# Kernel optimization log

Measured on AMD Instinct MI355X. Metric: run time of the kernel, lower is better.

The kernel has to match this reference:

```python
import jax, jax.numpy as jnp
import numpy as np

N = 50000      # nodes
E = 800000     # edges (before self-loops)
F_IN = 128     # num_features
HID = 32       # hidden_channels
HEADS = 4
CLS = 40       # num_classes
NEG_SLOPE = 0.2


def setup_inputs() -> dict:
    key = jax.random.key(0)
    ks = jax.random.split(key, 10)
    s = 0.1
    x = jax.random.normal(ks[0], (N, F_IN), jnp.float32)
    edge_index = jax.random.randint(ks[1], (2, E), 0, N, jnp.int32)
    W1 = jax.random.normal(ks[2], (F_IN, HEADS * HID), jnp.float32) * s
    att_src1 = jax.random.normal(ks[3], (HEADS, HID), jnp.float32) * s
    att_dst1 = jax.random.normal(ks[4], (HEADS, HID), jnp.float32) * s
    b1 = jnp.zeros((HEADS * HID,), jnp.float32)
    W2 = jax.random.normal(ks[5], (HEADS * HID, CLS), jnp.float32) * s
    att_src2 = jax.random.normal(ks[6], (1, CLS), jnp.float32) * s
    att_dst2 = jax.random.normal(ks[7], (1, CLS), jnp.float32) * s
    b2 = jnp.zeros((CLS,), jnp.float32)
    return {"x": x, "edge_index": edge_index,
            "W1": W1, "att_src1": att_src1, "att_dst1": att_dst1, "b1": b1,
            "W2": W2, "att_src2": att_src2, "att_dst2": att_dst2, "b2": b2}


def gat_layer(x, src, dst, W, a_src, a_dst, b, concat):
    """PyG GATConv: per-head linear, edge attention logits a_src.h_j + a_dst.h_i,
    LeakyReLU, segment softmax over incoming edges per dst, weighted scatter-sum."""
    n = x.shape[0]
    H, C = a_src.shape
    h = (x @ W).reshape(n, H, C)                       # [N, H, C]
    al_s = jnp.einsum('nhc,hc->nh', h, a_src)          # [N, H]
    al_d = jnp.einsum('nhc,hc->nh', h, a_dst)          # [N, H]
    e = jax.nn.leaky_relu(al_s[src] + al_d[dst], NEG_SLOPE)  # [E, H]
    e_max = jax.lax.stop_gradient(jax.ops.segment_max(e, dst, num_segments=n))
    e = jnp.exp(e - e_max[dst])
    denom = jax.ops.segment_sum(e, dst, num_segments=n)      # [N, H]
    alpha = e / (denom[dst] + 1e-16)                         # [E, H]
    out = jax.ops.segment_sum(h[src] * alpha[:, :, None], dst, num_segments=n)  # [N, H, C]
    out = out.reshape(n, H * C) if concat else out.mean(axis=1)
    return out + b


def reference(x, edge_index, W1, att_src1, att_dst1, b1, W2, att_src2, att_dst2, b2):
    n = x.shape[0]
    loops = jnp.arange(n, dtype=edge_index.dtype)
    src = jnp.concatenate([edge_index[0], loops])  # PyG adds self-loops by default
    dst = jnp.concatenate([edge_index[1], loops])
    h = gat_layer(x, src, dst, W1, att_src1, att_dst1, b1, concat=True)
    h = jax.nn.relu(h)  # dropout is identity in eval mode
    h = gat_layer(h, src, dst, W2, att_src2, att_dst2, b2, concat=False)
    return jax.nn.log_softmax(h, axis=1)
```

## Files before the change

### kernel.cpp

```cpp
#include <hip/hip_runtime.h>
#include <hip/hip_bf16.h>
#include <cstdint>
#include <cstddef>

#define NN 50000
#define EE 800000
#define FIN 128
#define D1 128
#define HEADS 4
#define HID 32
#define CLS 40
#define NEG 0.2f
#define MAXDEG 64
#define P2 128
#define PSZ2 391
#define CAP 8192
#define ABLK 400
#define ASLICE 500
#define GEMM1B 391

typedef __attribute__((ext_vector_type(8))) short short8;
typedef __attribute__((ext_vector_type(4))) float float4v;
typedef __attribute__((ext_vector_type(2))) float float2v;

union U16 { uint4 u; short8 s; };

__device__ __forceinline__ float bf2f(unsigned short u) {
    union { unsigned int i; float f; } v; v.i = ((unsigned int)u) << 16; return v.f;
}
__device__ __forceinline__ unsigned short f2bf(float f) {
    union { unsigned int i; float f; } v; v.f = f;
    unsigned int r = v.i + 0x7fffu + ((v.i >> 16) & 1u);
    return (unsigned short)(r >> 16);
}
__device__ __forceinline__ float2v up2(unsigned int u) {
    union { unsigned int i; float f; } lo, hi;
    lo.i = u << 16; hi.i = u & 0xffff0000u;
    float2v r; r[0] = lo.f; r[1] = hi.f; return r;
}

__global__ __launch_bounds__(256) void bucket_k(const int* __restrict__ eidx,
                                                unsigned int* __restrict__ seg,
                                                int* __restrict__ seg_cnt) {
    __shared__ int hist[P2], base_s[P2], run[P2];
    int t = threadIdx.x;
    if (t < P2) { hist[t] = 0; run[t] = 0; }
    __syncthreads();
    const int4* dst4 = (const int4*)(eidx + EE);
    const int4* src4 = (const int4*)eidx;
    int i0 = blockIdx.x * ASLICE;
    for (int i = i0 + t; i < i0 + ASLICE; i += 256) {
        int4 d = dst4[i];
        atomicAdd(&hist[d.x / PSZ2], 1);
        atomicAdd(&hist[d.y / PSZ2], 1);
        atomicAdd(&hist[d.z / PSZ2], 1);
        atomicAdd(&hist[d.w / PSZ2], 1);
    }
    __syncthreads();
    if (t < P2) base_s[t] = (hist[t] > 0) ? atomicAdd(&seg_cnt[t], hist[t]) : 0;
    __syncthreads();
    for (int i = i0 + t; i < i0 + ASLICE; i += 256) {
        int4 d = dst4[i];
        int4 s = src4[i];
        int p, off, idx;
        p = d.x / PSZ2; off = atomicAdd(&run[p], 1); idx = base_s[p] + off;
        if (idx < CAP) seg[(size_t)p * CAP + idx] = ((unsigned)s.x << 16) | (unsigned)(d.x - p * PSZ2);
        p = d.y / PSZ2; off = atomicAdd(&run[p], 1); idx = base_s[p] + off;
        if (idx < CAP) seg[(size_t)p * CAP + idx] = ((unsigned)s.y << 16) | (unsigned)(d.y - p * PSZ2);
        p = d.z / PSZ2; off = atomicAdd(&run[p], 1); idx = base_s[p] + off;
        if (idx < CAP) seg[(size_t)p * CAP + idx] = ((unsigned)s.z << 16) | (unsigned)(d.z - p * PSZ2);
        p = d.w / PSZ2; off = atomicAdd(&run[p], 1); idx = base_s[p] + off;
        if (idx < CAP) seg[(size_t)p * CAP + idx] = ((unsigned)s.w << 16) | (unsigned)(d.w - p * PSZ2);
    }
}

union BSM {
    struct { uint4 Wl[2048]; float sas[128]; float sad[128]; } g;
    int hist[PSZ2];
};

__global__ __launch_bounds__(256, 4) void bg_k(const unsigned int* __restrict__ seg,
                                               const int* __restrict__ seg_cnt,
                                               int* __restrict__ cnt,
                                               unsigned short* __restrict__ ssrcp,
                                               const float* __restrict__ X,
                                               const float* __restrict__ W,
                                               const float* __restrict__ as1,
                                               const float* __restrict__ ad1,
                                               unsigned int* __restrict__ H1b,
                                               float* __restrict__ ALS1,
                                               float* __restrict__ ALD1) {
    __shared__ BSM sm;
    int t = threadIdx.x;

    if (blockIdx.x < P2) {
        int p = blockIdx.x;
        int lo = p * PSZ2;
        int psz = min(PSZ2, NN - lo);
        for (int i = t; i < psz; i += 256) {
            sm.hist[i] = 1;
            ssrcp[(size_t)(lo + i) * MAXDEG] = (unsigned short)(lo + i);
        }
        __syncthreads();
        int m = min(seg_cnt[p], CAP);
        const unsigned int* sp = seg + (size_t)p * CAP;
        for (int i = t; i < m; i += 256) {
            unsigned int pr = sp[i];
            int dl  = (int)(pr & 0xffffu);
            int src = (int)(pr >> 16);
            int slot = atomicAdd(&sm.hist[dl], 1);
            if (slot < MAXDEG) ssrcp[(size_t)(lo + dl) * MAXDEG + slot] = (unsigned short)src;
        }
        __syncthreads();
        for (int i = t; i < psz; i += 256) cnt[lo + i] = sm.hist[i];
        return;
    }

    int bI = blockIdx.x - P2;
    if (t < 128) { sm.g.sas[t] = as1[t]; sm.g.sad[t] = ad1[t]; }
    for (int g = t; g < 2048; g += 256) {
        int ct = g >> 8, rem = g & 255, kc = rem >> 6, l = rem & 63;
        int c = ct * 16 + (l & 15);
        int k0 = kc * 32 + (l >> 4) * 8;
        U16 u;
#pragma unroll
        for (int j = 0; j < 8; j++) u.s[j] = (short)f2bf(W[(k0 + j) * D1 + c]);
        sm.g.Wl[g] = u.u;
    }
    __syncthreads();

    int wid = t >> 6, lane = t & 63, quad = lane >> 4, lrow = lane & 15;
    int wrow0 = bI * 128 + wid * 32;

    short8 afr[2][4];
#pragma unroll
    for (int rt = 0; rt < 2; rt++) {
        int r = wrow0 + rt * 16 + lrow;
#pragma unroll
        for (int kc = 0; kc < 4; kc++) {
            short8 a = {0, 0, 0, 0, 0, 0, 0, 0};
            if (r < NN) {
                const float* xp = X + (size_t)r * FIN + kc * 32 + quad * 8;
                float4 x0 = *(const float4*)xp;
                float4 x1 = *(const float4*)(xp + 4);
                a[0] = (short)f2bf(x0.x); a[1] = (short)f2bf(x0.y);
                a[2] = (short)f2bf(x0.z); a[3] = (short)f2bf(x0.w);
                a[4] = (short)f2bf(x1.x); a[5] = (short)f2bf(x1.y);
                a[6] = (short)f2bf(x1.z); a[7] = (short)f2bf(x1.w);
            }
            afr[rt][kc] = a;
        }
    }

    float4v acc[2][4];

    for (int cp = 0; cp < 2; ++cp) {
#pragma unroll
        for (int rt = 0; rt < 2; rt++)
#pragma unroll
            for (int c4 = 0; c4 < 4; c4++) acc[rt][c4] = (float4v)(0.f);

#pragma unroll
        for (int c4 = 0; c4 < 4; c4++) {
#pragma unroll
            for (int kc = 0; kc < 4; kc++) {
                U16 b; b.u = sm.g.Wl[((cp * 4 + c4) * 4 + kc) * 64 + lane];
                acc[0][c4] = __builtin_amdgcn_mfma_f32_16x16x32_bf16(afr[0][kc], b.s, acc[0][c4], 0, 0, 0);
                acc[1][c4] = __builtin_amdgcn_mfma_f32_16x16x32_bf16(afr[1][kc], b.s, acc[1][c4], 0, 0, 0);
            }
        }

#pragma unroll
        for (int rt = 0; rt < 2; rt++) {
#pragma unroll
            for (int reg = 0; reg < 4; reg++) {
                float ps[2] = {0.f, 0.f};
                float pd[2] = {0.f, 0.f};
#pragma unroll
                for (int c4 = 0; c4 < 4; c4++) {
                    float v = acc[rt][c4][reg];
                    int ct = cp * 4 + c4;
                    ps[c4 >> 1] += v * sm.g.sas[ct * 16 + lrow];
                    pd[c4 >> 1] += v * sm.g.sad[ct * 16 + lrow];
                }
#pragma unroll
                for (int o = 1; o < 16; o <<= 1) {
#pragma unroll
                    for (int h = 0; h < 2; h++) {
                        ps[h] += __shfl_xor(ps[h], o);
                        pd[h] += __shfl_xor(pd[h], o);
                    }
                }
                int r = wrow0 + rt * 16 + quad * 4 + reg;
                if (lrow == 0 && r < NN) {
                    *(float2*)&ALS1[(size_t)r * 4 + cp * 2] = make_float2(ps[0], ps[1]);
                    *(float2*)&ALD1[(size_t)r * 4 + cp * 2] = make_float2(pd[0], pd[1]);
                }
            }
        }

#pragma unroll
        for (int rt = 0; rt < 2; rt++)
#pragma unroll
            for (int c4 = 0; c4 < 4; c4++)
#pragma unroll
                for (int reg = 0; reg < 4; reg++) {
                    float v = acc[rt][c4][reg];
                    float o = __shfl_xor(v, 1);
                    int r = wrow0 + rt * 16 + quad * 4 + reg;
                    if (((lane & 1) == 0) && r < NN) {
                        unsigned int u = (unsigned int)f2bf(v) | ((unsigned int)f2bf(o) << 16);
                        H1b[(size_t)r * 64 + (cp * 4 + c4) * 8 + (lrow >> 1)] = u;
                    }
                }
    }
}

__global__ __launch_bounds__(256) void gather1_k(const int* __restrict__ cnt,
                                                 const unsigned short* __restrict__ ssrcp,
                                                 const uint4* __restrict__ H1b4,
                                                 const float4* __restrict__ ALS,
                                                 const float4* __restrict__ ALD,
                                                 const float* __restrict__ b1,
                                                 uint4* __restrict__ OUT1b4) {
    __shared__ float wlds[4][MAXDEG][4];
    __shared__ int sidlds[4][MAXDEG];
    int wid = threadIdx.x >> 6, lane = threadIdx.x & 63;
    int v = blockIdx.x * 4 + wid;
    int deg = min(cnt[v], MAXDEG);
    float4 ad = ALD[v];
    float w0 = 0.f, w1 = 0.f, w2 = 0.f, w3 = 0.f;
    if (lane < deg) {
        int s = (int)ssrcp[(size_t)v * MAXDEG + lane];
        sidlds[wid][lane] = s;
        float4 as = ALS[s];
        float l0 = as.x + ad.x; l0 = l0 > 0.f ? l0 : NEG * l0;
        float l1 = as.y + ad.y; l1 = l1 > 0.f ? l1 : NEG * l1;
        float l2 = as.z + ad.z; l2 = l2 > 0.f ? l2 : NEG * l2;
        float l3 = as.w + ad.w; l3 = l3 > 0.f ? l3 : NEG * l3;
        w0 = __expf(l0); w1 = __expf(l1); w2 = __expf(l2); w3 = __expf(l3);
        wlds[wid][lane][0] = w0; wlds[wid][lane][1] = w1;
        wlds[wid][lane][2] = w2; wlds[wid][lane][3] = w3;
    }
    float d0 = w0, d1 = w1, d2 = w2, d3 = w3;
#pragma unroll
    for (int o = 1; o < 64; o <<= 1) {
        d0 += __shfl_xor(d0, o); d1 += __shfl_xor(d1, o);
        d2 += __shfl_xor(d2, o); d3 += __shfl_xor(d3, o);
    }
    __syncthreads();
    int g = lane >> 4, l = lane & 15, head = l >> 2;
    float2v A0 = {0.f, 0.f}, A1 = {0.f, 0.f}, A2 = {0.f, 0.f}, A3 = {0.f, 0.f};
    {
        int j = g;
        bool valid = j < deg;
        float wj = 0.f; uint4 q = {};
        if (valid) {
            wj = wlds[wid][j][head];
            q = H1b4[(size_t)sidlds[wid][j] * 16 + l];
        }
        while (valid) {
            int jn = j + 4;
            bool vn = jn < deg;
            float wn = 0.f; uint4 qn = {};
            if (vn) {
                wn = wlds[wid][jn][head];
                qn = H1b4[(size_t)sidlds[wid][jn] * 16 + l];
            }
            float2v wv = {wj, wj};
            A0 += wv * up2(q.x);
            A1 += wv * up2(q.y);
            A2 += wv * up2(q.z);
            A3 += wv * up2(q.w);
            j = jn; valid = vn; wj = wn; q = qn;
        }
    }
    float a0 = A0[0], a1 = A0[1], a2 = A1[0], a3 = A1[1];
    float a4 = A2[0], a5 = A2[1], a6 = A3[0], a7 = A3[1];
#pragma unroll
    for (int o = 16; o < 64; o <<= 1) {
        a0 += __shfl_xor(a0, o); a1 += __shfl_xor(a1, o);
        a2 += __shfl_xor(a2, o); a3 += __shfl_xor(a3, o);
        a4 += __shfl_xor(a4, o); a5 += __shfl_xor(a5, o);
        a6 += __shfl_xor(a6, o); a7 += __shfl_xor(a7, o);
    }
    if (lane < 16) {
        float den = (head == 0) ? d0 : (head == 1) ? d1 : (head == 2) ? d2 : d3;
        den += 1e-16f;
        float4 bA = *(const float4*)&b1[8 * l];
        float4 bB = *(const float4*)&b1[8 * l + 4];
        float o0 = fmaxf(a0 / den + bA.x, 0.f);
        float o1 = fmaxf(a1 / den + bA.y, 0.f);
        float o2 = fmaxf(a2 / den + bA.z, 0.f);
        float o3 = fmaxf(a3 / den + bA.w, 0.f);
        float o4 = fmaxf(a4 / den + bB.x, 0.f);
        float o5 = fmaxf(a5 / den + bB.y, 0.f);
        float o6 = fmaxf(a6 / den + bB.z, 0.f);
        float o7 = fmaxf(a7 / den + bB.w, 0.f);
        uint4 u;
        u.x = (unsigned int)f2bf(o0) | ((unsigned int)f2bf(o1) << 16);
        u.y = (unsigned int)f2bf(o2) | ((unsigned int)f2bf(o3) << 16);
        u.z = (unsigned int)f2bf(o4) | ((unsigned int)f2bf(o5) << 16);
        u.w = (unsigned int)f2bf(o6) | ((unsigned int)f2bf(o7) << 16);
        OUT1b4[(size_t)v * 16 + l] = u;
    }
}

__global__ __launch_bounds__(256) void gemm2_k(const unsigned int* __restrict__ OUT1b,
                                               const float* __restrict__ W2,
                                               const float* __restrict__ as2,
                                               const float* __restrict__ ad2,
                                               unsigned int* __restrict__ H2b,
                                               float* __restrict__ ALS2,
                                               float* __restrict__ ALD2) {
    __shared__ uint4 Wl[768];
    __shared__ float sas[48], sad[48];
    int t = threadIdx.x;
    if (t < 48) {
        sas[t] = (t < CLS) ? as2[t] : 0.f;
        sad[t] = (t < CLS) ? ad2[t] : 0.f;
    }
    for (int g = t; g < 768; g += 256) {
        int ct = g >> 8, rem = g & 255, kc = rem >> 6, l = rem & 63;
        int c = ct * 16 + (l & 15);
        int k0 = kc * 32 + (l >> 4) * 8;
        U16 u;
#pragma unroll
        for (int j = 0; j < 8; j++)
            u.s[j] = (c < CLS) ? (short)f2bf(W2[(k0 + j) * CLS + c]) : (short)0;
        Wl[g] = u.u;
    }
    __syncthreads();

    int wid = t >> 6, lane = t & 63, quad = lane >> 4, lrow = lane & 15;
    int wrow0 = blockIdx.x * 128 + wid * 32;

    U16 afr[2][4];
#pragma unroll
    for (int rt = 0; rt < 2; rt++) {
        int r = wrow0 + rt * 16 + lrow;
#pragma unroll
        for (int kc = 0; kc < 4; kc++) {
            if (r < NN)
                afr[rt][kc].u = ((const uint4*)OUT1b)[(size_t)r * 16 + kc * 4 + quad];
            else
                afr[rt][kc].u = make_uint4(0, 0, 0, 0);
        }
    }

    float4v acc[2][3];
#pragma unroll
    for (int rt = 0; rt < 2; rt++)
#pragma unroll
        for (int ct = 0; ct < 3; ct++) acc[rt][ct] = (float4v)(0.f);

#pragma unroll
    for (int ct = 0; ct < 3; ct++) {
#pragma unroll
        for (int kc = 0; kc < 4; kc++) {
            U16 b; b.u = Wl[(ct * 4 + kc) * 64 + lane];
            acc[0][ct] = __builtin_amdgcn_mfma_f32_16x16x32_bf16(afr[0][kc].s, b.s, acc[0][ct], 0, 0, 0);
            acc[1][ct] = __builtin_amdgcn_mfma_f32_16x16x32_bf16(afr[1][kc].s, b.s, acc[1][ct], 0, 0, 0);
        }
    }

#pragma unroll
    for (int rt = 0; rt < 2; rt++) {
#pragma unroll
        for (int reg = 0; reg < 4; reg++) {
            float ps = 0.f, pd = 0.f;
#pragma unroll
            for (int ct = 0; ct < 3; ct++) {
                float v = acc[rt][ct][reg];
                ps += v * sas[ct * 16 + lrow];
                pd += v * sad[ct * 16 + lrow];
            }
#pragma unroll
            for (int o = 1; o < 16; o <<= 1) {
                ps += __shfl_xor(ps, o);
                pd += __shfl_xor(pd, o);
            }
            int r = wrow0 + rt * 16 + quad * 4 + reg;
            if (lrow == 0 && r < NN) {
                ALS2[r] = ps;
                ALD2[r] = pd;
            }
        }
    }

#pragma unroll
    for (int rt = 0; rt < 2; rt++)
#pragma unroll
        for (int ct = 0; ct < 3; ct++)
#pragma unroll
            for (int reg = 0; reg < 4; reg++) {
                float v = acc[rt][ct][reg];
                float o = __shfl_xor(v, 1);
                int r = wrow0 + rt * 16 + quad * 4 + reg;
                int c = ct * 16 + lrow;
                if (((lane & 1) == 0) && c < CLS && r < NN) {
                    unsigned int u = (unsigned int)f2bf(v) | ((unsigned int)f2bf(o) << 16);
                    H2b[(size_t)r * 20 + (c >> 1)] = u;
                }
            }
}

__global__ __launch_bounds__(256) void gather2_k(const int* __restrict__ cnt,
                                                 const unsigned short* __restrict__ ssrcp,
                                                 const unsigned int* __restrict__ H2b,
                                                 const float* __restrict__ ALS,
                                                 const float* __restrict__ ALD,
                                                 const float* __restrict__ b2,
                                                 float* __restrict__ out) {
    int wid = threadIdx.x >> 6, t = threadIdx.x & 63;
    int v = blockIdx.x * 4 + wid;
    int deg = min(cnt[v], MAXDEG);
    __shared__ float w[4][MAXDEG];
    __shared__ int sid[4][MAXDEG];
    __shared__ float part[4][3][CLS];
    float den = 0.f;
    float adv = ALD[v];
    if (t < deg) {
        int s = (int)ssrcp[(size_t)v * MAXDEG + t];
        sid[wid][t] = s;
        float l = ALS[s] + adv; l = l > 0.f ? l : NEG * l;
        float e = __expf(l);
        w[wid][t] = e; den = e;
    }
    __syncthreads();
    int g = t / 20, c = t % 20;
    if (t < 60) {
        float2v A = {0.f, 0.f};
        int j = g;
        bool valid = j < deg;
        float wj = 0.f; unsigned int u = 0u;
        if (valid) { wj = w[wid][j]; u = H2b[(size_t)sid[wid][j] * 20 + c]; }
        while (valid) {
            int jn = j + 3;
            bool vn = jn < deg;
            float wn = 0.f; unsigned int un = 0u;
            if (vn) { wn = w[wid][jn]; un = H2b[(size_t)sid[wid][jn] * 20 + c]; }
            float2v wv = {wj, wj};
            A += wv * up2(u);
            j = jn; valid = vn; wj = wn; u = un;
        }
        part[wid][g][2 * c] = A[0];
        part[wid][g][2 * c + 1] = A[1];
    }
#pragma unroll
    for (int o = 32; o > 0; o >>= 1) den += __shfl_xor(den, o);
    __syncthreads();
    float z = (t < CLS) ? (part[wid][0][t] + part[wid][1][t] + part[wid][2][t]) / (den + 1e-16f) + b2[t]
                        : -1e30f;
    float mx = z;
#pragma unroll
    for (int o = 32; o > 0; o >>= 1) mx = fmaxf(mx, __shfl_xor(mx, o));
    float ex = (t < CLS) ? __expf(z - mx) : 0.f;
    float se = ex;
#pragma unroll
    for (int o = 32; o > 0; o >>= 1) se += __shfl_xor(se, o);
    if (t < CLS) out[(size_t)v * CLS + t] = z - mx - __logf(se);
}

extern "C" void kernel_launch(void* const* d_in, const int* in_sizes, int n_in,
                              void* d_out, int out_size, void* d_ws, size_t ws_size,
                              hipStream_t stream) {
    const float* x   = (const float*)d_in[0];
    const int*   eix = (const int*)d_in[1];
    const float* W1  = (const float*)d_in[2];
    const float* as1 = (const float*)d_in[3];
    const float* ad1 = (const float*)d_in[4];
    const float* b1  = (const float*)d_in[5];
    const float* W2  = (const float*)d_in[6];
    const float* as2 = (const float*)d_in[7];
    const float* ad2 = (const float*)d_in[8];
    const float* b2  = (const float*)d_in[9];
    float* out = (float*)d_out;

    char* p = (char*)d_ws;
    auto carve = [&](size_t bytes) -> void* {
        void* r = (void*)p;
        p += (bytes + 255) & ~(size_t)255;
        return r;
    };
    unsigned int* H1b   = (unsigned int*)carve((size_t)NN * 64 * 4);
    unsigned int* OUT1b = (unsigned int*)carve((size_t)NN * 64 * 4);
    unsigned int* H2b   = (unsigned int*)carve((size_t)NN * 20 * 4);
    float* ALS1 = (float*)carve((size_t)NN * 4 * 4);
    float* ALD1 = (float*)carve((size_t)NN * 4 * 4);
    float* ALS2 = (float*)carve((size_t)NN * 4);
    float* ALD2 = (float*)carve((size_t)NN * 4);
    int* cnt    = (int*)carve((size_t)NN * 4);
    unsigned short* ssrcp = (unsigned short*)carve((size_t)NN * MAXDEG * 2);
    unsigned int* seg   = (unsigned int*)carve((size_t)P2 * CAP * 4);
    int* seg_cnt        = (int*)carve((size_t)P2 * 4);

    hipMemsetAsync(seg_cnt, 0, (size_t)P2 * 4, stream);

    bucket_k<<<ABLK, 256, 0, stream>>>(eix, seg, seg_cnt);
    bg_k<<<P2 + GEMM1B, 256, 0, stream>>>(seg, seg_cnt, cnt, ssrcp, x, W1, as1, ad1,
                                          H1b, ALS1, ALD1);
    gather1_k<<<NN / 4, 256, 0, stream>>>(cnt, ssrcp, (const uint4*)H1b,
                                          (const float4*)ALS1, (const float4*)ALD1,
                                          b1, (uint4*)OUT1b);
    gemm2_k<<<(NN + 127) / 128, 256, 0, stream>>>(OUT1b, W2, as2, ad2, H2b, ALS2, ALD2);
    gather2_k<<<NN / 4, 256, 0, stream>>>(cnt, ssrcp, H2b, ALS2, ALD2, b2, out);
}
```

Baseline: 208.1 us.

## Fuse layer-1 gather with layer-2 GEMM and drop seg_cnt memset

Merges the layer-1 attention gather and the layer-2 projection GEMM into one kernel: each block aggregates 16 nodes into LDS, then runs MFMA on them with W2 staged in LDS. This removes the OUT1b global round trip and one launch. It also moves the bucket counter to a device global that the consumer kernel resets, which drops the memset. In exchange, W2 is reloaded and converted per 16-node block (3125 blocks instead of 391), the GEMM tile is smaller, and only some waves do the epilogue work.

```diff
diff --git a/kernel.cpp b/kernel.cpp
--- a/kernel.cpp
+++ b/kernel.cpp
@@ -39,9 +39,10 @@
     float2v r; r[0] = lo.f; r[1] = hi.f; return r;
 }
 
+__device__ int g_seg_cnt[P2];
+
 __global__ __launch_bounds__(256) void bucket_k(const int* __restrict__ eidx,
-                                                unsigned int* __restrict__ seg,
-                                                int* __restrict__ seg_cnt) {
+                                                unsigned int* __restrict__ seg) {
     __shared__ int hist[P2], base_s[P2], run[P2];
     int t = threadIdx.x;
     if (t < P2) { hist[t] = 0; run[t] = 0; }
@@ -57,7 +58,7 @@
         atomicAdd(&hist[d.w / PSZ2], 1);
     }
     __syncthreads();
-    if (t < P2) base_s[t] = (hist[t] > 0) ? atomicAdd(&seg_cnt[t], hist[t]) : 0;
+    if (t < P2) base_s[t] = (hist[t] > 0) ? atomicAdd(&g_seg_cnt[t], hist[t]) : 0;
     __syncthreads();
     for (int i = i0 + t; i < i0 + ASLICE; i += 256) {
         int4 d = dst4[i];
@@ -80,7 +81,6 @@
 };
 
 __global__ __launch_bounds__(256, 4) void bg_k(const unsigned int* __restrict__ seg,
-                                               const int* __restrict__ seg_cnt,
                                                int* __restrict__ cnt,
                                                unsigned short* __restrict__ ssrcp,
                                                const float* __restrict__ X,
@@ -97,12 +97,13 @@
         int p = blockIdx.x;
         int lo = p * PSZ2;
         int psz = min(PSZ2, NN - lo);
+        int m = min(g_seg_cnt[p], CAP);
         for (int i = t; i < psz; i += 256) {
             sm.hist[i] = 1;
             ssrcp[(size_t)(lo + i) * MAXDEG] = (unsigned short)(lo + i);
         }
         __syncthreads();
-        int m = min(seg_cnt[p], CAP);
+        if (t == 0) g_seg_cnt[p] = 0;
         const unsigned int* sp = seg + (size_t)p * CAP;
         for (int i = t; i < m; i += 256) {
             unsigned int pr = sp[i];
@@ -216,162 +217,148 @@
     }
 }
 
-__global__ __launch_bounds__(256) void gather1_k(const int* __restrict__ cnt,
-                                                 const unsigned short* __restrict__ ssrcp,
-                                                 const uint4* __restrict__ H1b4,
-                                                 const float4* __restrict__ ALS,
-                                                 const float4* __restrict__ ALD,
-                                                 const float* __restrict__ b1,
-                                                 uint4* __restrict__ OUT1b4) {
-    __shared__ float wlds[4][MAXDEG][4];
-    __shared__ int sidlds[4][MAXDEG];
-    int wid = threadIdx.x >> 6, lane = threadIdx.x & 63;
-    int v = blockIdx.x * 4 + wid;
-    int deg = min(cnt[v], MAXDEG);
-    float4 ad = ALD[v];
-    float w0 = 0.f, w1 = 0.f, w2 = 0.f, w3 = 0.f;
-    if (lane < deg) {
-        int s = (int)ssrcp[(size_t)v * MAXDEG + lane];
-        sidlds[wid][lane] = s;
-        float4 as = ALS[s];
-        float l0 = as.x + ad.x; l0 = l0 > 0.f ? l0 : NEG * l0;
-        float l1 = as.y + ad.y; l1 = l1 > 0.f ? l1 : NEG * l1;
-        float l2 = as.z + ad.z; l2 = l2 > 0.f ? l2 : NEG * l2;
-        float l3 = as.w + ad.w; l3 = l3 > 0.f ? l3 : NEG * l3;
-        w0 = __expf(l0); w1 = __expf(l1); w2 = __expf(l2); w3 = __expf(l3);
-        wlds[wid][lane][0] = w0; wlds[wid][lane][1] = w1;
-        wlds[wid][lane][2] = w2; wlds[wid][lane][3] = w3;
-    }
-    float d0 = w0, d1 = w1, d2 = w2, d3 = w3;
-#pragma unroll
-    for (int o = 1; o < 64; o <<= 1) {
-        d0 += __shfl_xor(d0, o); d1 += __shfl_xor(d1, o);
-        d2 += __shfl_xor(d2, o); d3 += __shfl_xor(d3, o);
-    }
-    __syncthreads();
-    int g = lane >> 4, l = lane & 15, head = l >> 2;
-    float2v A0 = {0.f, 0.f}, A1 = {0.f, 0.f}, A2 = {0.f, 0.f}, A3 = {0.f, 0.f};
-    {
-        int j = g;
-        bool valid = j < deg;
-        float wj = 0.f; uint4 q = {};
-        if (valid) {
-            wj = wlds[wid][j][head];
-            q = H1b4[(size_t)sidlds[wid][j] * 16 + l];
-        }
-        while (valid) {
-            int jn = j + 4;
-            bool vn = jn < deg;
-            float wn = 0.f; uint4 qn = {};
-            if (vn) {
-                wn = wlds[wid][jn][head];
-                qn = H1b4[(size_t)sidlds[wid][jn] * 16 + l];
-            }
-            float2v wv = {wj, wj};
-            A0 += wv * up2(q.x);
-            A1 += wv * up2(q.y);
-            A2 += wv * up2(q.z);
-            A3 += wv * up2(q.w);
-            j = jn; valid = vn; wj = wn; q = qn;
-        }
-    }
-    float a0 = A0[0], a1 = A0[1], a2 = A1[0], a3 = A1[1];
-    float a4 = A2[0], a5 = A2[1], a6 = A3[0], a7 = A3[1];
-#pragma unroll
-    for (int o = 16; o < 64; o <<= 1) {
-        a0 += __shfl_xor(a0, o); a1 += __shfl_xor(a1, o);
-        a2 += __shfl_xor(a2, o); a3 += __shfl_xor(a3, o);
-        a4 += __shfl_xor(a4, o); a5 += __shfl_xor(a5, o);
-        a6 += __shfl_xor(a6, o); a7 += __shfl_xor(a7, o);
-    }
-    if (lane < 16) {
-        float den = (head == 0) ? d0 : (head == 1) ? d1 : (head == 2) ? d2 : d3;
-        den += 1e-16f;
-        float4 bA = *(const float4*)&b1[8 * l];
-        float4 bB = *(const float4*)&b1[8 * l + 4];
-        float o0 = fmaxf(a0 / den + bA.x, 0.f);
-        float o1 = fmaxf(a1 / den + bA.y, 0.f);
-        float o2 = fmaxf(a2 / den + bA.z, 0.f);
-        float o3 = fmaxf(a3 / den + bA.w, 0.f);
-        float o4 = fmaxf(a4 / den + bB.x, 0.f);
-        float o5 = fmaxf(a5 / den + bB.y, 0.f);
-        float o6 = fmaxf(a6 / den + bB.z, 0.f);
-        float o7 = fmaxf(a7 / den + bB.w, 0.f);
-        uint4 u;
-        u.x = (unsigned int)f2bf(o0) | ((unsigned int)f2bf(o1) << 16);
-        u.y = (unsigned int)f2bf(o2) | ((unsigned int)f2bf(o3) << 16);
-        u.z = (unsigned int)f2bf(o4) | ((unsigned int)f2bf(o5) << 16);
-        u.w = (unsigned int)f2bf(o6) | ((unsigned int)f2bf(o7) << 16);
-        OUT1b4[(size_t)v * 16 + l] = u;
-    }
-}
-
-__global__ __launch_bounds__(256) void gemm2_k(const unsigned int* __restrict__ OUT1b,
-                                               const float* __restrict__ W2,
-                                               const float* __restrict__ as2,
-                                               const float* __restrict__ ad2,
-                                               unsigned int* __restrict__ H2b,
-                                               float* __restrict__ ALS2,
-                                               float* __restrict__ ALD2) {
+__global__ __launch_bounds__(256) void g12_k(const int* __restrict__ cnt,
+                                             const unsigned short* __restrict__ ssrcp,
+                                             const uint4* __restrict__ H1b4,
+                                             const float4* __restrict__ ALS,
+                                             const float4* __restrict__ ALD,
+                                             const float* __restrict__ b1,
+                                             const float* __restrict__ W2,
+                                             const float* __restrict__ as2,
+                                             const float* __restrict__ ad2,
+                                             unsigned int* __restrict__ H2b,
+                                             float* __restrict__ ALS2,
+                                             float* __restrict__ ALD2) {
     __shared__ uint4 Wl[768];
     __shared__ float sas[48], sad[48];
+    __shared__ float wlds[4][MAXDEG][4];
+    __shared__ int   sidlds[4][MAXDEG];
+    __shared__ uint4 out1[16 * 17];
     int t = threadIdx.x;
     if (t < 48) {
         sas[t] = (t < CLS) ? as2[t] : 0.f;
         sad[t] = (t < CLS) ? ad2[t] : 0.f;
     }
-    for (int g = t; g < 768; g += 256) {
-        int ct = g >> 8, rem = g & 255, kc = rem >> 6, l = rem & 63;
+    for (int i = t; i < 768; i += 256) {
+        int ct = i >> 8, rem = i & 255, kc = rem >> 6, l = rem & 63;
         int c = ct * 16 + (l & 15);
         int k0 = kc * 32 + (l >> 4) * 8;
         U16 u;
 #pragma unroll
         for (int j = 0; j < 8; j++)
             u.s[j] = (c < CLS) ? (short)f2bf(W2[(k0 + j) * CLS + c]) : (short)0;
-        Wl[g] = u.u;
-    }
-    __syncthreads();
-
-    int wid = t >> 6, lane = t & 63, quad = lane >> 4, lrow = lane & 15;
-    int wrow0 = blockIdx.x * 128 + wid * 32;
-
-    U16 afr[2][4];
-#pragma unroll
-    for (int rt = 0; rt < 2; rt++) {
-        int r = wrow0 + rt * 16 + lrow;
-#pragma unroll
-        for (int kc = 0; kc < 4; kc++) {
-            if (r < NN)
-                afr[rt][kc].u = ((const uint4*)OUT1b)[(size_t)r * 16 + kc * 4 + quad];
-            else
-                afr[rt][kc].u = make_uint4(0, 0, 0, 0);
-        }
-    }
-
-    float4v acc[2][3];
-#pragma unroll
-    for (int rt = 0; rt < 2; rt++)
-#pragma unroll
-        for (int ct = 0; ct < 3; ct++) acc[rt][ct] = (float4v)(0.f);
-
-#pragma unroll
-    for (int ct = 0; ct < 3; ct++) {
+        Wl[i] = u.u;
+    }
+
+    int wid = t >> 6, lane = t & 63;
+    int vb = blockIdx.x * 16;
+
+    for (int pass = 0; pass < 4; ++pass) {
+        int v  = vb + pass * 4 + wid;
+        int nl = pass * 4 + wid;
+        int deg = min(cnt[v], MAXDEG);
+        float4 ad = ALD[v];
+        float w0 = 0.f, w1 = 0.f, w2 = 0.f, w3 = 0.f;
+        if (lane < deg) {
+            int s = (int)ssrcp[(size_t)v * MAXDEG + lane];
+            sidlds[wid][lane] = s;
+            float4 as = ALS[s];
+            float l0 = as.x + ad.x; l0 = l0 > 0.f ? l0 : NEG * l0;
+            float l1 = as.y + ad.y; l1 = l1 > 0.f ? l1 : NEG * l1;
+            float l2 = as.z + ad.z; l2 = l2 > 0.f ? l2 : NEG * l2;
+            float l3 = as.w + ad.w; l3 = l3 > 0.f ? l3 : NEG * l3;
+            w0 = __expf(l0); w1 = __expf(l1); w2 = __expf(l2); w3 = __expf(l3);
+            wlds[wid][lane][0] = w0; wlds[wid][lane][1] = w1;
+            wlds[wid][lane][2] = w2; wlds[wid][lane][3] = w3;
+        }
+        float d0 = w0, d1 = w1, d2 = w2, d3 = w3;
+#pragma unroll
+        for (int o = 1; o < 64; o <<= 1) {
+            d0 += __shfl_xor(d0, o); d1 += __shfl_xor(d1, o);
+            d2 += __shfl_xor(d2, o); d3 += __shfl_xor(d3, o);
+        }
+        int g = lane >> 4, l = lane & 15, head = l >> 2;
+        float2v A0 = {0.f, 0.f}, A1 = {0.f, 0.f}, A2 = {0.f, 0.f}, A3 = {0.f, 0.f};
+        {
+            int j = g;
+            bool valid = j < deg;
+            float wj = 0.f; uint4 q = {};
+            if (valid) {
+                wj = wlds[wid][j][head];
+                q = H1b4[(size_t)sidlds[wid][j] * 16 + l];
+            }
+            while (valid) {
+                int jn = j + 4;
+                bool vn = jn < deg;
+                float wn = 0.f; uint4 qn = {};
+                if (vn) {
+                    wn = wlds[wid][jn][head];
+                    qn = H1b4[(size_t)sidlds[wid][jn] * 16 + l];
+                }
+                float2v wv = {wj, wj};
+                A0 += wv * up2(q.x);
+                A1 += wv * up2(q.y);
+                A2 += wv * up2(q.z);
+                A3 += wv * up2(q.w);
+                j = jn; valid = vn; wj = wn; q = qn;
+            }
+        }
+        float a0 = A0[0], a1 = A0[1], a2 = A1[0], a3 = A1[1];
+        float a4 = A2[0], a5 = A2[1], a6 = A3[0], a7 = A3[1];
+#pragma unroll
+        for (int o = 16; o < 64; o <<= 1) {
+            a0 += __shfl_xor(a0, o); a1 += __shfl_xor(a1, o);
+            a2 += __shfl_xor(a2, o); a3 += __shfl_xor(a3, o);
+            a4 += __shfl_xor(a4, o); a5 += __shfl_xor(a5, o);
+            a6 += __shfl_xor(a6, o); a7 += __shfl_xor(a7, o);
+        }
+        if (lane < 16) {
+            float den = (head == 0) ? d0 : (head == 1) ? d1 : (head == 2) ? d2 : d3;
+            den += 1e-16f;
+            float4 bA = *(const float4*)&b1[8 * l];
+            float4 bB = *(const float4*)&b1[8 * l + 4];
+            float o0 = fmaxf(a0 / den + bA.x, 0.f);
+            float o1 = fmaxf(a1 / den + bA.y, 0.f);
+            float o2 = fmaxf(a2 / den + bA.z, 0.f);
+            float o3 = fmaxf(a3 / den + bA.w, 0.f);
+            float o4 = fmaxf(a4 / den + bB.x, 0.f);
+            float o5 = fmaxf(a5 / den + bB.y, 0.f);
+            float o6 = fmaxf(a6 / den + bB.z, 0.f);
+            float o7 = fmaxf(a7 / den + bB.w, 0.f);
+            uint4 u;
+            u.x = (unsigned int)f2bf(o0) | ((unsigned int)f2bf(o1) << 16);
+            u.y = (unsigned int)f2bf(o2) | ((unsigned int)f2bf(o3) << 16);
+            u.z = (unsigned int)f2bf(o4) | ((unsigned int)f2bf(o5) << 16);
+            u.w = (unsigned int)f2bf(o6) | ((unsigned int)f2bf(o7) << 16);
+            out1[nl * 17 + l] = u;
+        }
+    }
+    __syncthreads();
+
+    int quad = lane >> 4, lrow = lane & 15;
+    U16 afr[4];
+#pragma unroll
+    for (int kc = 0; kc < 4; kc++)
+        afr[kc].u = out1[lrow * 17 + kc * 4 + quad];
+
+    float4v acc[3];
+#pragma unroll
+    for (int ct = 0; ct < 3; ct++) acc[ct] = (float4v)(0.f);
+#pragma unroll
+    for (int ct = 0; ct < 3; ct++)
 #pragma unroll
         for (int kc = 0; kc < 4; kc++) {
             U16 b; b.u = Wl[(ct * 4 + kc) * 64 + lane];
-            acc[0][ct] = __builtin_amdgcn_mfma_f32_16x16x32_bf16(afr[0][kc].s, b.s, acc[0][ct], 0, 0, 0);
-            acc[1][ct] = __builtin_amdgcn_mfma_f32_16x16x32_bf16(afr[1][kc].s, b.s, acc[1][ct], 0, 0, 0);
-        }
-    }
-
-#pragma unroll
-    for (int rt = 0; rt < 2; rt++) {
+            acc[ct] = __builtin_amdgcn_mfma_f32_16x16x32_bf16(afr[kc].s, b.s, acc[ct], 0, 0, 0);
+        }
+
+    if (wid == 3) {
 #pragma unroll
         for (int reg = 0; reg < 4; reg++) {
             float ps = 0.f, pd = 0.f;
 #pragma unroll
             for (int ct = 0; ct < 3; ct++) {
-                float v = acc[rt][ct][reg];
+                float v = acc[ct][reg];
                 ps += v * sas[ct * 16 + lrow];
                 pd += v * sad[ct * 16 + lrow];
             }
@@ -380,29 +367,26 @@
                 ps += __shfl_xor(ps, o);
                 pd += __shfl_xor(pd, o);
             }
-            int r = wrow0 + rt * 16 + quad * 4 + reg;
-            if (lrow == 0 && r < NN) {
+            int r = vb + quad * 4 + reg;
+            if (lrow == 0) {
                 ALS2[r] = ps;
                 ALD2[r] = pd;
             }
         }
-    }
-
-#pragma unroll
-    for (int rt = 0; rt < 2; rt++)
-#pragma unroll
-        for (int ct = 0; ct < 3; ct++)
-#pragma unroll
-            for (int reg = 0; reg < 4; reg++) {
-                float v = acc[rt][ct][reg];
-                float o = __shfl_xor(v, 1);
-                int r = wrow0 + rt * 16 + quad * 4 + reg;
-                int c = ct * 16 + lrow;
-                if (((lane & 1) == 0) && c < CLS && r < NN) {
-                    unsigned int u = (unsigned int)f2bf(v) | ((unsigned int)f2bf(o) << 16);
-                    H2b[(size_t)r * 20 + (c >> 1)] = u;
-                }
-            }
+    } else {
+        int ct = wid;
+#pragma unroll
+        for (int reg = 0; reg < 4; reg++) {
+            float v = acc[ct][reg];
+            float o = __shfl_xor(v, 1);
+            int r = vb + quad * 4 + reg;
+            int c = ct * 16 + lrow;
+            if (((lane & 1) == 0) && c < CLS) {
+                unsigned int u = (unsigned int)f2bf(v) | ((unsigned int)f2bf(o) << 16);
+                H2b[(size_t)r * 20 + (c >> 1)] = u;
+            }
+        }
+    }
 }
 
 __global__ __launch_bounds__(256) void gather2_k(const int* __restrict__ cnt,
@@ -484,7 +468,6 @@
         return r;
     };
     unsigned int* H1b   = (unsigned int*)carve((size_t)NN * 64 * 4);
-    unsigned int* OUT1b = (unsigned int*)carve((size_t)NN * 64 * 4);
     unsigned int* H2b   = (unsigned int*)carve((size_t)NN * 20 * 4);
     float* ALS1 = (float*)carve((size_t)NN * 4 * 4);
     float* ALD1 = (float*)carve((size_t)NN * 4 * 4);
@@ -493,16 +476,12 @@
     int* cnt    = (int*)carve((size_t)NN * 4);
     unsigned short* ssrcp = (unsigned short*)carve((size_t)NN * MAXDEG * 2);
     unsigned int* seg   = (unsigned int*)carve((size_t)P2 * CAP * 4);
-    int* seg_cnt        = (int*)carve((size_t)P2 * 4);
-
-    hipMemsetAsync(seg_cnt, 0, (size_t)P2 * 4, stream);
-
-    bucket_k<<<ABLK, 256, 0, stream>>>(eix, seg, seg_cnt);
-    bg_k<<<P2 + GEMM1B, 256, 0, stream>>>(seg, seg_cnt, cnt, ssrcp, x, W1, as1, ad1,
+
+    bucket_k<<<ABLK, 256, 0, stream>>>(eix, seg);
+    bg_k<<<P2 + GEMM1B, 256, 0, stream>>>(seg, cnt, ssrcp, x, W1, as1, ad1,
                                           H1b, ALS1, ALD1);
-    gather1_k<<<NN / 4, 256, 0, stream>>>(cnt, ssrcp, (const uint4*)H1b,
-                                          (const float4*)ALS1, (const float4*)ALD1,
-                                          b1, (uint4*)OUT1b);
-    gemm2_k<<<(NN + 127) / 128, 256, 0, stream>>>(OUT1b, W2, as2, ad2, H2b, ALS2, ALD2);
+    g12_k<<<NN / 16, 256, 0, stream>>>(cnt, ssrcp, (const uint4*)H1b,
+                                       (const float4*)ALS1, (const float4*)ALD1,
+                                       b1, W2, as2, ad2, H2b, ALS2, ALD2);
     gather2_k<<<NN / 4, 256, 0, stream>>>(cnt, ssrcp, H2b, ALS2, ALD2, b2, out);
 }
```

New measurement: 221.4 us. +6.4%, slower.
